# Optimization experiments

Hardware: AMD Instinct MI355X
Metric: run time of the kernel (lower is better)

Reference implementation:

```python
import jax, jax.numpy as jnp
import numpy as np

N_POS = 8
POS_W = jnp.array([0.95, 0.9, 0.85, 0.5, 0.4, 0.2, 0.15, 0.05], dtype=jnp.float32)
EVENT_HORIZON = 0.1

L, D = 4096, 2048


def setup_inputs() -> dict:
    key = jax.random.key(0)
    ks = jax.random.split(key, 10)
    token_vecs = jax.random.normal(ks[0], (L, D), dtype=jnp.float32)
    pos_idx = jax.random.randint(ks[1], (L,), 0, 8)
    depth = jax.random.randint(ks[2], (L,), 0, 12)
    token_pos = jnp.arange(L, dtype=jnp.int64) if jax.config.jax_enable_x64 else jnp.arange(L, dtype=jnp.int32)
    slot_idx = jax.random.randint(ks[3], (L,), 0, 16)
    confidences = jax.random.uniform(ks[4], (L,), dtype=jnp.float32)
    sun_resonances = jax.random.uniform(ks[5], (L,), dtype=jnp.float32)
    # learned parameters (match torch init)
    G_micro = jnp.full((N_POS, N_POS), 0.1, dtype=jnp.float32)
    G_macro = jnp.array(0.5, dtype=jnp.float32)
    k_spring = jnp.full((N_POS,), 0.05, dtype=jnp.float32)
    temperature = jnp.array(1.0, dtype=jnp.float32)
    Wv_w = jax.random.normal(ks[6], (D, D), dtype=jnp.float32) * 0.02
    Wv_b = jnp.zeros((D,), dtype=jnp.float32)
    Wo_w = jax.random.normal(ks[7], (D, D), dtype=jnp.float32) * 0.02
    Wo_b = jnp.zeros((D,), dtype=jnp.float32)
    return dict(token_vecs=token_vecs, pos_idx=pos_idx, depth=depth,
                token_pos=token_pos, slot_idx=slot_idx, confidences=confidences,
                sun_resonances=sun_resonances, G_micro=G_micro, G_macro=G_macro,
                k_spring=k_spring, temperature=temperature, Wv_w=Wv_w, Wv_b=Wv_b,
                Wo_w=Wo_w, Wo_b=Wo_b)


def _scores(token_vecs, pos_idx, depth, token_pos, slot_idx, confidences,
            sun_resonances, G_micro, G_macro, k_spring):
    n = token_vecs.shape[0]
    p = pos_idx % N_POS
    # semantic mass: ||v|| detached in torch (.item()), POS weight, (1 + resonance)
    norms = jax.lax.stop_gradient(jnp.linalg.norm(token_vecs, axis=-1))
    res = jax.lax.stop_gradient(sun_resonances)
    conf = jax.lax.stop_gradient(confidences)
    m = norms * POS_W[p] * (1.0 + res)                     # [L]
    mm = m[:, None] * m[None, :]                            # [L, L]
    # micro gravity: per-POS-pair G over squared slot distance (min 1)
    slot_d = jnp.abs(slot_idx[:, None] - slot_idx[None, :])
    r_slot = jnp.maximum(slot_d, 1).astype(jnp.float32)
    f_micro = jax.nn.sigmoid(G_micro)[p[:, None], p[None, :]] * mm / (r_slot * r_slot)
    # macro gravity over orbital (depth) distance
    r_orb = (jnp.abs(depth[:, None] - depth[None, :]) + 1).astype(jnp.float32)
    f_macro = jax.nn.sigmoid(G_macro) * mm / (r_orb * r_orb)
    # spring force grows with token distance, k indexed by row POS
    tok_d = jnp.abs(token_pos[:, None] - token_pos[None, :]).astype(jnp.float32)
    f_spring = jax.nn.sigmoid(k_spring)[p][:, None] * tok_d
    # black hole force
    collapsed = conf <= EVENT_HORIZON
    gap = jnp.where(collapsed, 1.0, conf - EVENT_HORIZON)
    bh = jnp.where(collapsed, -1e6, -0.01 / (gap * gap))    # [L]
    total = f_micro + f_macro + f_spring + bh[:, None] + bh[None, :]
    eye = jnp.eye(n, dtype=bool)
    row_skip = (bh < -1e5)[:, None]                          # collapsed rows stay zero
    return jnp.where(row_skip | eye, 0.0, total)


def reference(token_vecs, pos_idx, depth, token_pos, slot_idx, confidences,
              sun_resonances, G_micro, G_macro, k_spring, temperature,
              Wv_w, Wv_b, Wo_w, Wo_b):
    scores = _scores(token_vecs, pos_idx, depth, token_pos, slot_idx,
                     confidences, sun_resonances, G_micro, G_macro, k_spring)
    T = jnp.maximum(jnp.abs(temperature), 0.1)
    A = jax.nn.softmax(scores / T, axis=-1)
    V = token_vecs @ Wv_w.T + Wv_b
    out = (A @ V) @ Wo_w.T + Wo_b
    return out, A, scores
```

## Files before the change

### kernel.cpp

```cpp
#include <hip/hip_runtime.h>
#include <math.h>

#define LL 4096
#define DD 2048

typedef __attribute__((ext_vector_type(8))) short short8;
typedef __attribute__((ext_vector_type(4))) float f32x4;
typedef unsigned int u32;
typedef unsigned short u16;

__device__ __constant__ float POS_W_c[8] = {0.95f, 0.9f, 0.85f, 0.5f, 0.4f, 0.2f, 0.15f, 0.05f};

static __device__ inline u32 f2bf(float f) {
    u32 u = __builtin_bit_cast(u32, f);
    return (u + 0x7fffu + ((u >> 16) & 1u)) >> 16;
}
static __device__ inline u32 cvt2_bf16(float a, float b) {
    return f2bf(a) | (f2bf(b) << 16);
}
static __device__ inline short8 pack8_bf16(float4 a, float4 b) {
    uint4 u = make_uint4(cvt2_bf16(a.x, a.y), cvt2_bf16(a.z, a.w),
                         cvt2_bf16(b.x, b.y), cvt2_bf16(b.z, b.w));
    return __builtin_bit_cast(short8, u);
}
static __device__ inline void glds16(const u16* g, u16* l) {
    __builtin_amdgcn_global_load_lds(
        (const __attribute__((address_space(1))) void*)g,
        (__attribute__((address_space(3))) void*)l, 16, 0, 0);
}

__global__ __launch_bounds__(256) void f32_to_bf16_k(
    const float* __restrict__ in, u16* __restrict__ out, int n8)
{
    int idx = blockIdx.x * 256 + threadIdx.x;
    int stride = gridDim.x * 256;
    for (int i = idx; i < n8; i += stride) {
        const float4* p = (const float4*)(in + (size_t)i * 8);
        float4 a = p[0], b = p[1];
        *(short8*)(out + (size_t)i * 8) = pack8_bf16(a, b);
    }
}

__global__ __launch_bounds__(256) void row_stats_k(
    const float* __restrict__ tv, const int* __restrict__ pos_idx,
    const float* __restrict__ conf, const float* __restrict__ res,
    const float* __restrict__ k_spring,
    float* __restrict__ m_arr, float* __restrict__ bh_arr,
    float* __restrict__ spring_arr, int* __restrict__ coll_arr)
{
    int i = blockIdx.x;
    int t = threadIdx.x;
    const float4* row = (const float4*)(tv + (size_t)i * DD);
    float s = 0.0f;
#pragma unroll
    for (int c = 0; c < 2; ++c) {
        float4 v = row[t + c * 256];
        s += v.x * v.x + v.y * v.y + v.z * v.z + v.w * v.w;
    }
#pragma unroll
    for (int o = 32; o; o >>= 1) s += __shfl_xor(s, o);
    __shared__ float tmp[4];
    if ((t & 63) == 0) tmp[t >> 6] = s;
    __syncthreads();
    if (t == 0) {
        float tot = tmp[0] + tmp[1] + tmp[2] + tmp[3];
        float norm = sqrtf(tot);
        int p = pos_idx[i] & 7;
        float m = norm * POS_W_c[p] * (1.0f + res[i]);
        float cf = conf[i];
        bool col = (cf <= 0.1f);
        float gap = col ? 1.0f : (cf - 0.1f);
        float bh = col ? -1e6f : (-0.01f / (gap * gap));
        m_arr[i] = m;
        bh_arr[i] = bh;
        coll_arr[i] = (bh < -1e5f) ? 1 : 0;
        spring_arr[i] = 1.0f / (1.0f + __expf(-k_spring[p]));
    }
}

__global__ __launch_bounds__(256) void scores_k(
    const int* __restrict__ pos_idx, const int* __restrict__ depth,
    const int* __restrict__ token_pos, const int* __restrict__ slot_idx,
    const float* __restrict__ m_arr, const float* __restrict__ bh_arr,
    const float* __restrict__ spring_arr, const int* __restrict__ coll_arr,
    const float* __restrict__ G_micro, const float* __restrict__ G_macro,
    const float* __restrict__ temperature,
    float* __restrict__ scores, float* __restrict__ Amat,
    u16* __restrict__ Ab)
{
    int i = blockIdx.x;
    int t = threadIdx.x;
    int lane = t & 63, wid = t >> 6;

    __shared__ float sigG[64];
    __shared__ float red[4];
    if (t < 64) sigG[t] = 1.0f / (1.0f + __expf(-G_micro[t]));
    __syncthreads();

    float sGmac = 1.0f / (1.0f + __expf(-G_macro[0]));
    float T = fmaxf(fabsf(temperature[0]), 0.1f);
    float invT = 1.0f / T;

    int pi = pos_idx[i] & 7;
    float mi = m_arr[i];
    float bhi = bh_arr[i];
    float spr = spring_arr[i];
    int sloti = slot_idx[i], depi = depth[i], tpi = token_pos[i];
    bool rowskip = (coll_arr[i] != 0);

    float* srow = scores + (size_t)i * LL;
    float* arow = Amat + (size_t)i * LL;
    u16* abrow = Ab + (size_t)i * LL;

    float x[16];
    float xmax = -3.4e38f;
#pragma unroll
    for (int c = 0; c < 16; ++c) {
        int j = t + c * 256;
        float s = 0.0f;
        if (!rowskip && j != i) {
            float mj = m_arr[j];
            float mm = mi * mj;
            int pj = pos_idx[j] & 7;
            int sd = abs(sloti - slot_idx[j]); if (sd < 1) sd = 1;
            float rs = (float)sd;
            float fmic = sigG[pi * 8 + pj] * mm * __builtin_amdgcn_rcpf(rs * rs);
            int od = abs(depi - depth[j]) + 1;
            float ro = (float)od;
            float fmac = sGmac * mm * __builtin_amdgcn_rcpf(ro * ro);
            float td = fabsf((float)(tpi - token_pos[j]));
            s = fmic + fmac + spr * td + bhi + bh_arr[j];
        }
        srow[j] = s;
        x[c] = s * invT;
        xmax = fmaxf(xmax, x[c]);
    }
#pragma unroll
    for (int o = 32; o; o >>= 1) xmax = fmaxf(xmax, __shfl_xor(xmax, o));
    if (lane == 0) red[wid] = xmax;
    __syncthreads();
    xmax = fmaxf(fmaxf(red[0], red[1]), fmaxf(red[2], red[3]));
    __syncthreads();
    float e[16];
    float esum = 0.0f;
#pragma unroll
    for (int c = 0; c < 16; ++c) {
        e[c] = __expf(x[c] - xmax);
        esum += e[c];
    }
#pragma unroll
    for (int o = 32; o; o >>= 1) esum += __shfl_xor(esum, o);
    if (lane == 0) red[wid] = esum;
    __syncthreads();
    float inv = 1.0f / (red[0] + red[1] + red[2] + red[3]);
#pragma unroll
    for (int c = 0; c < 16; ++c) {
        float a = e[c] * inv;
        arow[t + c * 256] = a;
        abrow[t + c * 256] = (u16)f2bf(a);
    }
}

template <int BIAS, int OUT_BF16>
__global__ __launch_bounds__(256) void gemm_db_k(
    const u16* __restrict__ Ap, const u16* __restrict__ Bp,
    const float* __restrict__ bias, void* __restrict__ Cp,
    int M, int N, int K, int gx)
{
    __shared__ __align__(1024) u16 lds[2][32][512];

    int t = threadIdx.x;
    int wid = t >> 6, lane = t & 63;
    int wm = wid >> 1, wn = wid & 1;
    int r = lane & 15, bq = lane >> 4;

    int sq = blockIdx.x & 7;
    int insq = blockIdx.x >> 3;
    int nsqx = gx >> 3;
    int sqy = sq / nsqx, sqx = sq - sqy * nsqx;
    int by = sqy * 8 + (insq >> 3);
    int bx = sqx * 8 + (insq & 7);
    int blockM = by * 128, blockN = bx * 128;

    f32x4 acc[4][4];
#pragma unroll
    for (int a = 0; a < 4; ++a)
#pragma unroll
        for (int b = 0; b < 4; ++b) acc[a][b] = (f32x4){0.f, 0.f, 0.f, 0.f};

    const u16* gsrc[8];
    u16* ldst[8];
#pragma unroll
    for (int i = 0; i < 8; ++i) {
        int c = wid * 8 + i;
        int cc = c & 15;
        int h = cc >> 3, s = cc & 7;
        const u16* base = (c >> 4)
            ? Bp + (size_t)(blockN + s * 16 + r) * K
            : Ap + (size_t)(blockM + s * 16 + r) * K;
        gsrc[i] = base + h * 32 + bq * 8;
        ldst[i] = &lds[0][c][0];
    }

    int nt = K >> 6;
#pragma unroll
    for (int i = 0; i < 8; ++i) glds16(gsrc[i], ldst[i]);

    for (int tt = 0; tt < nt; ++tt) {
        int cur = tt & 1;
        if (tt + 1 < nt) {
            int kt = (tt + 1) << 6;
            int bofs = (cur ^ 1) * 16384;
#pragma unroll
            for (int i = 0; i < 8; ++i) glds16(gsrc[i] + kt, ldst[i] + bofs);
            __builtin_amdgcn_sched_barrier(0);
            asm volatile("s_waitcnt vmcnt(8)" ::: "memory");
        } else {
            __builtin_amdgcn_sched_barrier(0);
            asm volatile("s_waitcnt vmcnt(0)" ::: "memory");
        }
        __builtin_amdgcn_sched_barrier(0);
        __builtin_amdgcn_s_barrier();
        __builtin_amdgcn_sched_barrier(0);

#pragma unroll
        for (int h = 0; h < 2; ++h) {
            short8 aF[4], bF[4];
#pragma unroll
            for (int mi = 0; mi < 4; ++mi)
                aF[mi] = *(const short8*)&lds[cur][h * 8 + wm * 4 + mi][lane * 8];
#pragma unroll
            for (int ni = 0; ni < 4; ++ni)
                bF[ni] = *(const short8*)&lds[cur][16 + h * 8 + wn * 4 + ni][lane * 8];
#pragma unroll
            for (int mi = 0; mi < 4; ++mi)
#pragma unroll
                for (int ni = 0; ni < 4; ++ni)
                    acc[mi][ni] = __builtin_amdgcn_mfma_f32_16x16x32_bf16(aF[mi], bF[ni], acc[mi][ni], 0, 0, 0);
        }
        __builtin_amdgcn_sched_barrier(0);
        __builtin_amdgcn_s_barrier();
        __builtin_amdgcn_sched_barrier(0);
    }

#pragma unroll
    for (int mi = 0; mi < 4; ++mi) {
        int rowb = blockM + wm * 64 + mi * 16 + bq * 4;
#pragma unroll
        for (int ni = 0; ni < 4; ++ni) {
            int col = blockN + wn * 64 + ni * 16 + r;
#pragma unroll
            for (int q = 0; q < 4; ++q) {
                float v = acc[mi][ni][q];
                int row = rowb + q;
                if (BIAS == 1) v += bias[row];
                else if (BIAS == 2) v += bias[col];
                if (OUT_BF16) {
                    ((u16*)Cp)[(size_t)row * N + col] = (u16)f2bf(v);
                } else {
                    ((float*)Cp)[(size_t)row * N + col] = v;
                }
            }
        }
    }
}

extern "C" void kernel_launch(void* const* d_in, const int* in_sizes, int n_in,
                              void* d_out, int out_size, void* d_ws, size_t ws_size,
                              hipStream_t stream) {
    (void)in_sizes; (void)n_in; (void)out_size; (void)ws_size;
    const float* tv        = (const float*)d_in[0];
    const int* pos_idx     = (const int*)d_in[1];
    const int* depth       = (const int*)d_in[2];
    const int* token_pos   = (const int*)d_in[3];
    const int* slot_idx    = (const int*)d_in[4];
    const float* conf      = (const float*)d_in[5];
    const float* res       = (const float*)d_in[6];
    const float* G_micro   = (const float*)d_in[7];
    const float* G_macro   = (const float*)d_in[8];
    const float* k_spring  = (const float*)d_in[9];
    const float* temperature = (const float*)d_in[10];
    const float* Wv_w      = (const float*)d_in[11];
    const float* Wv_b      = (const float*)d_in[12];
    const float* Wo_w      = (const float*)d_in[13];
    const float* Wo_b      = (const float*)d_in[14];

    float* out    = (float*)d_out;
    float* Amat   = out + (size_t)LL * DD;
    float* scores = Amat + (size_t)LL * LL;

    u16* Ab = (u16*)out;

    u16* VT  = (u16*)d_ws;
    u16* H   = VT + (size_t)DD * LL;
    u16* tvb = H + (size_t)LL * DD;
    u16* Wvb = tvb + (size_t)LL * DD;
    u16* Wob = Wvb + (size_t)DD * DD;
    float* m_arr      = (float*)(Wob + (size_t)DD * DD);
    float* bh_arr     = m_arr + LL;
    float* spring_arr = bh_arr + LL;
    int*   coll_arr   = (int*)(spring_arr + LL);

    f32_to_bf16_k<<<2048, 256, 0, stream>>>(tv, tvb, LL * DD / 8);
    f32_to_bf16_k<<<1024, 256, 0, stream>>>(Wv_w, Wvb, DD * DD / 8);
    f32_to_bf16_k<<<1024, 256, 0, stream>>>(Wo_w, Wob, DD * DD / 8);

    row_stats_k<<<LL, 256, 0, stream>>>(tv, pos_idx, conf, res, k_spring,
                                        m_arr, bh_arr, spring_arr, coll_arr);

    scores_k<<<LL, 256, 0, stream>>>(pos_idx, depth, token_pos, slot_idx,
                                     m_arr, bh_arr, spring_arr, coll_arr,
                                     G_micro, G_macro, temperature,
                                     scores, Amat, Ab);

    gemm_db_k<1, 1><<<512, 256, 0, stream>>>(Wvb, tvb, Wv_b, VT, DD, LL, DD, LL / 128);

    gemm_db_k<0, 1><<<512, 256, 0, stream>>>(Ab, VT, nullptr, H, LL, DD, LL, DD / 128);

    gemm_db_k<2, 0><<<512, 256, 0, stream>>>(H, Wob, Wo_b, out, LL, DD, DD, DD / 128);
}
```

Measured before the change: 511.7 us.

## Use four-stage LDS pipeline in GEMM and fuse token bf16 cast into row stats

The GEMM kernel moves from a double-buffered K=64 stage with two barriers per iteration to a four-buffer ring of K=32 stages, keeping three tile loads in flight and needing only one barrier per iteration. The aim is to hide global-to-LDS latency better and cut barrier stalls. The standalone fp32-to-bf16 conversion of token_vecs is folded into row_stats_k, which already reads each row, so one kernel launch and one full read pass go away. In exchange, each iteration does half as many MFMAs per barrier, and the LDS footprint stays at 64KB.

```diff
diff --git a/kernel.cpp b/kernel.cpp
--- a/kernel.cpp
+++ b/kernel.cpp
@@ -45,18 +45,17 @@
     const float* __restrict__ tv, const int* __restrict__ pos_idx,
     const float* __restrict__ conf, const float* __restrict__ res,
     const float* __restrict__ k_spring,
+    u16* __restrict__ tvb,
     float* __restrict__ m_arr, float* __restrict__ bh_arr,
     float* __restrict__ spring_arr, int* __restrict__ coll_arr)
 {
     int i = blockIdx.x;
     int t = threadIdx.x;
     const float4* row = (const float4*)(tv + (size_t)i * DD);
-    float s = 0.0f;
-#pragma unroll
-    for (int c = 0; c < 2; ++c) {
-        float4 v = row[t + c * 256];
-        s += v.x * v.x + v.y * v.y + v.z * v.z + v.w * v.w;
-    }
+    float4 a = row[t * 2], b = row[t * 2 + 1];
+    *(short8*)(tvb + (size_t)i * DD + t * 8) = pack8_bf16(a, b);
+    float s = a.x * a.x + a.y * a.y + a.z * a.z + a.w * a.w
+            + b.x * b.x + b.y * b.y + b.z * b.z + b.w * b.w;
 #pragma unroll
     for (int o = 32; o; o >>= 1) s += __shfl_xor(s, o);
     __shared__ float tmp[4];
@@ -162,12 +161,12 @@
 }
 
 template <int BIAS, int OUT_BF16>
-__global__ __launch_bounds__(256) void gemm_db_k(
+__global__ __launch_bounds__(256) void gemm_p4_k(
     const u16* __restrict__ Ap, const u16* __restrict__ Bp,
     const float* __restrict__ bias, void* __restrict__ Cp,
     int M, int N, int K, int gx)
 {
-    __shared__ __align__(1024) u16 lds[2][32][512];
+    __shared__ __align__(1024) u16 ldsF[4 * 16 * 512];
 
     int t = threadIdx.x;
     int wid = t >> 6, lane = t & 63;
@@ -188,59 +187,55 @@
 #pragma unroll
         for (int b = 0; b < 4; ++b) acc[a][b] = (f32x4){0.f, 0.f, 0.f, 0.f};
 
-    const u16* gsrc[8];
-    u16* ldst[8];
-#pragma unroll
-    for (int i = 0; i < 8; ++i) {
-        int c = wid * 8 + i;
-        int cc = c & 15;
-        int h = cc >> 3, s = cc & 7;
-        const u16* base = (c >> 4)
+    const u16* gsrc[4];
+    u16* ldst[4];
+#pragma unroll
+    for (int i = 0; i < 4; ++i) {
+        int c = wid * 4 + i;
+        int s = c & 7;
+        const u16* base = (c >> 3)
             ? Bp + (size_t)(blockN + s * 16 + r) * K
             : Ap + (size_t)(blockM + s * 16 + r) * K;
-        gsrc[i] = base + h * 32 + bq * 8;
-        ldst[i] = &lds[0][c][0];
-    }
-
-    int nt = K >> 6;
-#pragma unroll
-    for (int i = 0; i < 8; ++i) glds16(gsrc[i], ldst[i]);
+        gsrc[i] = base + bq * 8;
+        ldst[i] = &ldsF[c * 512];
+    }
+
+    int nt = K >> 5;
+#pragma unroll
+    for (int i = 0; i < 4; ++i) glds16(gsrc[i], ldst[i]);
+#pragma unroll
+    for (int i = 0; i < 4; ++i) glds16(gsrc[i] + 32, ldst[i] + 8192);
+#pragma unroll
+    for (int i = 0; i < 4; ++i) glds16(gsrc[i] + 64, ldst[i] + 16384);
 
     for (int tt = 0; tt < nt; ++tt) {
-        int cur = tt & 1;
-        if (tt + 1 < nt) {
-            int kt = (tt + 1) << 6;
-            int bofs = (cur ^ 1) * 16384;
-#pragma unroll
-            for (int i = 0; i < 8; ++i) glds16(gsrc[i] + kt, ldst[i] + bofs);
-            __builtin_amdgcn_sched_barrier(0);
-            asm volatile("s_waitcnt vmcnt(8)" ::: "memory");
-        } else {
-            __builtin_amdgcn_sched_barrier(0);
-            asm volatile("s_waitcnt vmcnt(0)" ::: "memory");
-        }
+        if (tt + 2 < nt)      asm volatile("s_waitcnt vmcnt(8)" ::: "memory");
+        else if (tt + 1 < nt) asm volatile("s_waitcnt vmcnt(4)" ::: "memory");
+        else                  asm volatile("s_waitcnt vmcnt(0)" ::: "memory");
         __builtin_amdgcn_sched_barrier(0);
         __builtin_amdgcn_s_barrier();
         __builtin_amdgcn_sched_barrier(0);
 
-#pragma unroll
-        for (int h = 0; h < 2; ++h) {
-            short8 aF[4], bF[4];
-#pragma unroll
-            for (int mi = 0; mi < 4; ++mi)
-                aF[mi] = *(const short8*)&lds[cur][h * 8 + wm * 4 + mi][lane * 8];
+        if (tt + 3 < nt) {
+            int kt = (tt + 3) << 5;
+            int bofs = ((tt + 3) & 3) * 8192;
+#pragma unroll
+            for (int i = 0; i < 4; ++i) glds16(gsrc[i] + kt, ldst[i] + bofs);
+        }
+
+        int cb = (tt & 3) * 8192;
+        short8 aF[4], bF[4];
+#pragma unroll
+        for (int mi = 0; mi < 4; ++mi)
+            aF[mi] = *(const short8*)&ldsF[cb + (wm * 4 + mi) * 512 + lane * 8];
+#pragma unroll
+        for (int ni = 0; ni < 4; ++ni)
+            bF[ni] = *(const short8*)&ldsF[cb + (8 + wn * 4 + ni) * 512 + lane * 8];
+#pragma unroll
+        for (int mi = 0; mi < 4; ++mi)
 #pragma unroll
             for (int ni = 0; ni < 4; ++ni)
-                bF[ni] = *(const short8*)&lds[cur][16 + h * 8 + wn * 4 + ni][lane * 8];
-#pragma unroll
-            for (int mi = 0; mi < 4; ++mi)
-#pragma unroll
-                for (int ni = 0; ni < 4; ++ni)
-                    acc[mi][ni] = __builtin_amdgcn_mfma_f32_16x16x32_bf16(aF[mi], bF[ni], acc[mi][ni], 0, 0, 0);
-        }
-        __builtin_amdgcn_sched_barrier(0);
-        __builtin_amdgcn_s_barrier();
-        __builtin_amdgcn_sched_barrier(0);
+                acc[mi][ni] = __builtin_amdgcn_mfma_f32_16x16x32_bf16(aF[mi], bF[ni], acc[mi][ni], 0, 0, 0);
     }
 
 #pragma unroll
@@ -301,21 +296,20 @@
     float* spring_arr = bh_arr + LL;
     int*   coll_arr   = (int*)(spring_arr + LL);
 
-    f32_to_bf16_k<<<2048, 256, 0, stream>>>(tv, tvb, LL * DD / 8);
     f32_to_bf16_k<<<1024, 256, 0, stream>>>(Wv_w, Wvb, DD * DD / 8);
     f32_to_bf16_k<<<1024, 256, 0, stream>>>(Wo_w, Wob, DD * DD / 8);
 
     row_stats_k<<<LL, 256, 0, stream>>>(tv, pos_idx, conf, res, k_spring,
-                                        m_arr, bh_arr, spring_arr, coll_arr);
+                                        tvb, m_arr, bh_arr, spring_arr, coll_arr);
 
     scores_k<<<LL, 256, 0, stream>>>(pos_idx, depth, token_pos, slot_idx,
                                      m_arr, bh_arr, spring_arr, coll_arr,
                                      G_micro, G_macro, temperature,
                                      scores, Amat, Ab);
 
-    gemm_db_k<1, 1><<<512, 256, 0, stream>>>(Wvb, tvb, Wv_b, VT, DD, LL, DD, LL / 128);
-
-    gemm_db_k<0, 1><<<512, 256, 0, stream>>>(Ab, VT, nullptr, H, LL, DD, LL, DD / 128);
-
-    gemm_db_k<2, 0><<<512, 256, 0, stream>>>(H, Wob, Wo_b, out, LL, DD, DD, DD / 128);
-}
+    gemm_p4_k<1, 1><<<512, 256, 0, stream>>>(Wvb, tvb, Wv_b, VT, DD, LL, DD, LL / 128);
+
+    gemm_p4_k<0, 1><<<512, 256, 0, stream>>>(Ab, VT, nullptr, H, LL, DD, LL, DD / 128);
+
+    gemm_p4_k<2, 0><<<512, 256, 0, stream>>>(H, Wob, Wo_b, out, LL, DD, DD, DD / 128);
+}
```

Measured after the change: 503.2 us. Within noise of the previous version (-1.7%).
